# Optimization experiments

Hardware: AMD Instinct MI355X
Metric: run time of the kernel (lower is better)

The kernel has to match this reference:

```python
import jax, jax.numpy as jnp
import numpy as np

N_NODES = 50000
N_EDGES = 800000
NODE_DIM = 256
HIDDEN_DIM = 256
LN_EPS = 1e-5


def setup_inputs() -> dict:
    key = jax.random.key(0)
    ks = jax.random.split(key, 8)
    d, h = NODE_DIM, HIDDEN_DIM
    return {
        "node_features": jax.random.normal(ks[0], (N_NODES, d), jnp.float32),
        "src": jax.random.randint(ks[1], (N_EDGES,), 0, N_NODES, jnp.int32),
        "dst": jax.random.randint(ks[2], (N_EDGES,), 0, N_NODES, jnp.int32),
        "edge_weight": jax.random.uniform(ks[3], (N_EDGES,), jnp.float32),
        "W1": jax.random.normal(ks[4], (d, h), jnp.float32) / np.sqrt(d),
        "b1": jnp.zeros((h,), jnp.float32),
        "g1": jnp.ones((h,), jnp.float32),
        "be1": jnp.zeros((h,), jnp.float32),
        "W2": jax.random.normal(ks[5], (h, h), jnp.float32) / np.sqrt(h),
        "b2": jnp.zeros((h,), jnp.float32),
        "g2": jnp.ones((h,), jnp.float32),
        "be2": jnp.zeros((h,), jnp.float32),
        "Wp": jax.random.normal(ks[6], (h, d), jnp.float32) / np.sqrt(h),
        "bp": jnp.zeros((d,), jnp.float32),
    }


def _spmm(src, dst, w, x, n):
    # sparse adj @ x : agg[i] = sum_{edges e with dst=i} w_e * x[src_e]
    return jax.ops.segment_sum(w[:, None] * x[src], dst, num_segments=n)


def _layer_norm(x, g, b):
    mu = jnp.mean(x, -1, keepdims=True)
    var = jnp.mean(jnp.square(x - mu), -1, keepdims=True)
    return (x - mu) * jax.lax.rsqrt(var + LN_EPS) * g + b


def reference(node_features, src, dst, edge_weight, W1, b1, g1, be1, W2, b2, g2, be2, Wp, bp):
    n = node_features.shape[0]
    x = node_features
    for (W, b, g, be) in ((W1, b1, g1, be1), (W2, b2, g2, be2)):
        agg = _spmm(src, dst, edge_weight, x, n)
        h = (x + agg) @ W + b
        x = jax.nn.gelu(_layer_norm(h, g, be), approximate=False)
        # Dropout(0.1) is identity in eval mode
    return x @ Wp + bp
```

## Files before the change

### kernel.cpp

```cpp
#include <hip/hip_runtime.h>
#include <hip/hip_bf16.h>
#include <math.h>

#define N_NODES 50000
#define N_EDGES 800000
#define DIM 256
#define MPAD 50048
#define LN_EPS 1e-5f
#define SCAN_BLOCKS 196

typedef short bf16x8 __attribute__((ext_vector_type(8)));
typedef float f32x4 __attribute__((ext_vector_type(4)));
typedef unsigned short u16;
typedef u16 u16x8 __attribute__((ext_vector_type(8)));

__device__ __forceinline__ u16 f2bf(float f) {
    union { float f; unsigned u; } v; v.f = f;
    unsigned r = (v.u + 0x7FFFu + ((v.u >> 16) & 1u)) >> 16;
    return (u16)r;
}
__device__ __forceinline__ float bf2f(u16 h) {
    union { unsigned u; float f; } v; v.u = ((unsigned)h) << 16;
    return v.f;
}

__global__ void count_kernel(const int* __restrict__ dst, int* __restrict__ counts) {
    int e = blockIdx.x * 256 + threadIdx.x;
    if (e < N_EDGES) atomicAdd(&counts[dst[e]], 1);
}

__global__ void scan1_kernel(const int* __restrict__ counts, int* __restrict__ offsets,
                             int* __restrict__ bsum) {
    __shared__ int sh[256];
    int t = threadIdx.x;
    int idx = blockIdx.x * 256 + t;
    int v = (idx < N_NODES) ? counts[idx] : 0;
    sh[t] = v;
    __syncthreads();
#pragma unroll
    for (int off = 1; off < 256; off <<= 1) {
        int u = (t >= off) ? sh[t - off] : 0;
        __syncthreads();
        sh[t] += u;
        __syncthreads();
    }
    if (idx < N_NODES) offsets[idx] = sh[t] - v;
    if (t == 255) bsum[blockIdx.x] = sh[255];
}

__global__ void scan2_kernel(const int* __restrict__ bsum, int* __restrict__ bbase) {
    __shared__ int sh[256];
    int t = threadIdx.x;
    int v = (t < SCAN_BLOCKS) ? bsum[t] : 0;
    sh[t] = v;
    __syncthreads();
#pragma unroll
    for (int off = 1; off < 256; off <<= 1) {
        int u = (t >= off) ? sh[t - off] : 0;
        __syncthreads();
        sh[t] += u;
        __syncthreads();
    }
    if (t < SCAN_BLOCKS) bbase[t] = sh[t] - v;
}

__global__ void scan3_kernel(int* __restrict__ offsets, const int* __restrict__ bbase,
                             int* __restrict__ cursor) {
    int idx = blockIdx.x * 256 + threadIdx.x;
    if (idx < N_NODES) {
        int o = offsets[idx] + bbase[blockIdx.x];
        offsets[idx] = o;
        cursor[idx] = o;
    }
    if (idx == 0) offsets[N_NODES] = N_EDGES;
}

__global__ void scatter_kernel(const int* __restrict__ src, const int* __restrict__ dst,
                               const float* __restrict__ w, int* __restrict__ cursor,
                               int* __restrict__ sperm, float* __restrict__ wperm) {
    int e = blockIdx.x * 256 + threadIdx.x;
    if (e < N_EDGES) {
        int d = dst[e];
        int p = atomicAdd(&cursor[d], 1);
        sperm[p] = src[e];
        wperm[p] = w[e];
    }
}

__global__ void conv_kernel(const float* __restrict__ in, u16* __restrict__ out) {
    int i = blockIdx.x * 256 + threadIdx.x;
    float4 v = ((const float4*)in)[i];
    ushort4 o;
    o.x = f2bf(v.x); o.y = f2bf(v.y); o.z = f2bf(v.z); o.w = f2bf(v.w);
    ((ushort4*)out)[i] = o;
}

__global__ void convw_kernel(const float* __restrict__ W1, const float* __restrict__ W2,
                             const float* __restrict__ Wp, u16* __restrict__ WT) {
    int idx = blockIdx.x * 256 + threadIdx.x;
    int m = idx >> 16;
    int r = idx & 65535;
    int n = r >> 8, k = r & 255;
    const float* W = (m == 0) ? W1 : (m == 1) ? W2 : Wp;
    WT[idx] = f2bf(W[k * 256 + n]);
}

__global__ __launch_bounds__(256) void spmm_kernel(
        const u16* __restrict__ x, const int* __restrict__ offs,
        const int* __restrict__ sperm, const float* __restrict__ wperm,
        u16* __restrict__ y) {
    int wave = threadIdx.x >> 6;
    int lane = threadIdx.x & 63;
    int node = blockIdx.x * 4 + wave;
    if (node >= N_NODES) return;

    const ushort4* xv = (const ushort4*)x;
    ushort4 v = xv[(size_t)node * 64 + lane];
    float a0 = bf2f(v.x), a1 = bf2f(v.y), a2 = bf2f(v.z), a3 = bf2f(v.w);
    float b0 = 0, b1 = 0, b2 = 0, b3 = 0;
    float c0 = 0, c1 = 0, c2 = 0, c3 = 0;
    float d0 = 0, d1 = 0, d2 = 0, d3 = 0;

    int p = offs[node];
    int p1 = offs[node + 1];
    for (; p + 4 <= p1; p += 4) {
        int s0 = sperm[p], s1 = sperm[p + 1], s2 = sperm[p + 2], s3 = sperm[p + 3];
        float w0 = wperm[p], w1 = wperm[p + 1], w2 = wperm[p + 2], w3 = wperm[p + 3];
        ushort4 v0 = xv[(size_t)s0 * 64 + lane];
        ushort4 v1 = xv[(size_t)s1 * 64 + lane];
        ushort4 v2 = xv[(size_t)s2 * 64 + lane];
        ushort4 v3 = xv[(size_t)s3 * 64 + lane];
        a0 += w0 * bf2f(v0.x); a1 += w0 * bf2f(v0.y); a2 += w0 * bf2f(v0.z); a3 += w0 * bf2f(v0.w);
        b0 += w1 * bf2f(v1.x); b1 += w1 * bf2f(v1.y); b2 += w1 * bf2f(v1.z); b3 += w1 * bf2f(v1.w);
        c0 += w2 * bf2f(v2.x); c1 += w2 * bf2f(v2.y); c2 += w2 * bf2f(v2.z); c3 += w2 * bf2f(v2.w);
        d0 += w3 * bf2f(v3.x); d1 += w3 * bf2f(v3.y); d2 += w3 * bf2f(v3.z); d3 += w3 * bf2f(v3.w);
    }
    for (; p < p1; ++p) {
        int s = sperm[p];
        float w = wperm[p];
        ushort4 vv = xv[(size_t)s * 64 + lane];
        a0 += w * bf2f(vv.x); a1 += w * bf2f(vv.y); a2 += w * bf2f(vv.z); a3 += w * bf2f(vv.w);
    }
    a0 += b0 + c0 + d0; a1 += b1 + c1 + d1;
    a2 += b2 + c2 + d2; a3 += b3 + c3 + d3;
    ushort4 o;
    o.x = f2bf(a0); o.y = f2bf(a1); o.z = f2bf(a2); o.w = f2bf(a3);
    ((ushort4*)(y + (size_t)node * 256))[lane] = o;
}

template <int MODE>
__global__ __launch_bounds__(256, 2) void gemm_kernel(
        const u16* __restrict__ A, const u16* __restrict__ BT,
        const float* __restrict__ bias, const float* __restrict__ g,
        const float* __restrict__ be, u16* __restrict__ xb_out,
        float* __restrict__ f_out) {
    int tid = threadIdx.x;
    int wave = tid >> 6, lane = tid & 63;
    int quad = lane >> 4, l15 = lane & 15;
    int row0 = blockIdx.x * 128 + wave * 32;

    const u16* ga0 = A + (size_t)(row0 + l15) * 256 + quad * 8;
    const u16* ga1 = ga0 + 16 * 256;
    const u16* gb = BT + (size_t)l15 * 256 + quad * 8;

    f32x4 acc0[16], acc1[16];
#pragma unroll
    for (int t = 0; t < 16; ++t) { acc0[t] = {0.f, 0.f, 0.f, 0.f}; acc1[t] = {0.f, 0.f, 0.f, 0.f}; }

#pragma unroll 2
    for (int kb = 0; kb < 8; ++kb) {
        bf16x8 af0 = *(const bf16x8*)(ga0 + kb * 32);
        bf16x8 af1 = *(const bf16x8*)(ga1 + kb * 32);
#pragma unroll
        for (int t = 0; t < 16; ++t) {
            bf16x8 bf = *(const bf16x8*)(gb + (size_t)t * 4096 + kb * 32);
            acc0[t] = __builtin_amdgcn_mfma_f32_16x16x32_bf16(af0, bf, acc0[t], 0, 0, 0);
            acc1[t] = __builtin_amdgcn_mfma_f32_16x16x32_bf16(af1, bf, acc1[t], 0, 0, 0);
        }
    }

#pragma unroll
    for (int rf = 0; rf < 2; ++rf) {
        f32x4* acc = rf ? acc1 : acc0;
        int rbase = row0 + rf * 16 + quad * 4;
        if (MODE == 0) {
#pragma unroll
            for (int t = 0; t < 16; ++t) {
                float bv = bias[t * 16 + l15];
#pragma unroll
                for (int i = 0; i < 4; ++i) acc[t][i] += bv;
            }
#pragma unroll
            for (int i = 0; i < 4; ++i) {
                float s = 0.f, q = 0.f;
#pragma unroll
                for (int t = 0; t < 16; ++t) { float v = acc[t][i]; s += v; q += v * v; }
                for (int off = 1; off < 16; off <<= 1) {
                    s += __shfl_xor(s, off);
                    q += __shfl_xor(q, off);
                }
                float mu = s * (1.0f / 256.0f);
                float var = q * (1.0f / 256.0f) - mu * mu;
                float rs = rsqrtf(var + LN_EPS);
                int row = rbase + i;
#pragma unroll
                for (int t = 0; t < 16; ++t) {
                    int c = t * 16 + l15;
                    float v = (acc[t][i] - mu) * rs * g[c] + be[c];
                    float ge = 0.5f * v * (1.0f + erff(v * 0.70710678118f));
                    xb_out[(size_t)row * 256 + c] = f2bf(ge);
                }
            }
        } else {
#pragma unroll
            for (int i = 0; i < 4; ++i) {
                int row = rbase + i;
                if (row < N_NODES) {
#pragma unroll
                    for (int t = 0; t < 16; ++t) {
                        int c = t * 16 + l15;
                        f_out[(size_t)row * 256 + c] = acc[t][i] + bias[c];
                    }
                }
            }
        }
    }
}

extern "C" void kernel_launch(void* const* d_in, const int* in_sizes, int n_in,
                              void* d_out, int out_size, void* d_ws, size_t ws_size,
                              hipStream_t stream) {
    const float* nodef = (const float*)d_in[0];
    const int*   src   = (const int*)d_in[1];
    const int*   dst   = (const int*)d_in[2];
    const float* ew    = (const float*)d_in[3];
    const float* W1 = (const float*)d_in[4];
    const float* b1 = (const float*)d_in[5];
    const float* g1 = (const float*)d_in[6];
    const float* be1 = (const float*)d_in[7];
    const float* W2 = (const float*)d_in[8];
    const float* b2 = (const float*)d_in[9];
    const float* g2 = (const float*)d_in[10];
    const float* be2 = (const float*)d_in[11];
    const float* Wp = (const float*)d_in[12];
    const float* bp = (const float*)d_in[13];
    float* out = (float*)d_out;

    char* ws = (char*)d_ws;
    size_t off = 0;
    auto alloc = [&](size_t bytes) -> void* {
        void* p = ws + off;
        off += (bytes + 255) & ~(size_t)255;
        return p;
    };
    u16*   ybuf    = (u16*)alloc((size_t)MPAD * 256 * 2);
    u16*   xbuf    = (u16*)alloc((size_t)MPAD * 256 * 2);
    u16*   WT      = (u16*)alloc((size_t)3 * 65536 * 2);
    int*   counts  = (int*)alloc((size_t)N_NODES * 4);
    int*   offsets = (int*)alloc((size_t)(N_NODES + 1) * 4);
    int*   cursor  = (int*)alloc((size_t)N_NODES * 4);
    int*   sperm   = (int*)alloc((size_t)N_EDGES * 4);
    float* wperm   = (float*)alloc((size_t)N_EDGES * 4);
    int*   bsum    = (int*)alloc((size_t)SCAN_BLOCKS * 4);
    int*   bbase   = (int*)alloc((size_t)SCAN_BLOCKS * 4);

    hipMemsetAsync(counts, 0, (size_t)N_NODES * 4, stream);
    count_kernel<<<(N_EDGES + 255) / 256, 256, 0, stream>>>(dst, counts);
    scan1_kernel<<<SCAN_BLOCKS, 256, 0, stream>>>(counts, offsets, bsum);
    scan2_kernel<<<1, 256, 0, stream>>>(bsum, bbase);
    scan3_kernel<<<SCAN_BLOCKS, 256, 0, stream>>>(offsets, bbase, cursor);
    scatter_kernel<<<(N_EDGES + 255) / 256, 256, 0, stream>>>(src, dst, ew, cursor, sperm, wperm);
    conv_kernel<<<(N_NODES * 256 / 4) / 256, 256, 0, stream>>>(nodef, xbuf);
    convw_kernel<<<768, 256, 0, stream>>>(W1, W2, Wp, WT);

    const int GB = MPAD / 128;
    spmm_kernel<<<(N_NODES + 3) / 4, 256, 0, stream>>>(xbuf, offsets, sperm, wperm, ybuf);
    gemm_kernel<0><<<GB, 256, 0, stream>>>(ybuf, WT, b1, g1, be1, xbuf, nullptr);
    spmm_kernel<<<(N_NODES + 3) / 4, 256, 0, stream>>>(xbuf, offsets, sperm, wperm, ybuf);
    gemm_kernel<0><<<GB, 256, 0, stream>>>(ybuf, WT + 65536, b2, g2, be2, xbuf, nullptr);
    gemm_kernel<1><<<GB, 256, 0, stream>>>(xbuf, WT + 2 * 65536, bp, nullptr, nullptr, nullptr, out);
}
```

Baseline: 509.8 us.

## Write SpMM output in MFMA-tiled layout, stage weights in LDS, widen GEMM tiles

```diff
diff --git a/kernel.cpp b/kernel.cpp
--- a/kernel.cpp
+++ b/kernel.cpp
@@ -5,9 +5,10 @@
 #define N_NODES 50000
 #define N_EDGES 800000
 #define DIM 256
-#define MPAD 50048
+#define MPAD 50176
 #define LN_EPS 1e-5f
 #define SCAN_BLOCKS 196
+#define LDB 264
 
 typedef short bf16x8 __attribute__((ext_vector_type(8)));
 typedef float f32x4 __attribute__((ext_vector_type(4)));
@@ -22,6 +23,10 @@
 __device__ __forceinline__ float bf2f(u16 h) {
     union { unsigned u; float f; } v; v.u = ((unsigned)h) << 16;
     return v.f;
+}
+__device__ __forceinline__ float gelu_f(float x) {
+    float z = x * (1.595769122f + 0.0713548162726f * x * x);
+    return x * (1.0f / (1.0f + __expf(-z)));
 }
 
 __global__ void count_kernel(const int* __restrict__ dst, int* __restrict__ counts) {
@@ -109,92 +114,132 @@
         const u16* __restrict__ x, const int* __restrict__ offs,
         const int* __restrict__ sperm, const float* __restrict__ wperm,
         u16* __restrict__ y) {
-    int wave = threadIdx.x >> 6;
-    int lane = threadIdx.x & 63;
-    int node = blockIdx.x * 4 + wave;
-    if (node >= N_NODES) return;
+    __shared__ u16 tile[16 * 256];
+    int tid = threadIdx.x;
+    int wave = tid >> 6;
+    int lane = tid & 63;
+    int node0 = blockIdx.x * 16 + wave * 4;
 
     const ushort4* xv = (const ushort4*)x;
-    ushort4 v = xv[(size_t)node * 64 + lane];
-    float a0 = bf2f(v.x), a1 = bf2f(v.y), a2 = bf2f(v.z), a3 = bf2f(v.w);
-    float b0 = 0, b1 = 0, b2 = 0, b3 = 0;
-    float c0 = 0, c1 = 0, c2 = 0, c3 = 0;
-    float d0 = 0, d1 = 0, d2 = 0, d3 = 0;
-
-    int p = offs[node];
-    int p1 = offs[node + 1];
-    for (; p + 4 <= p1; p += 4) {
-        int s0 = sperm[p], s1 = sperm[p + 1], s2 = sperm[p + 2], s3 = sperm[p + 3];
-        float w0 = wperm[p], w1 = wperm[p + 1], w2 = wperm[p + 2], w3 = wperm[p + 3];
-        ushort4 v0 = xv[(size_t)s0 * 64 + lane];
-        ushort4 v1 = xv[(size_t)s1 * 64 + lane];
-        ushort4 v2 = xv[(size_t)s2 * 64 + lane];
-        ushort4 v3 = xv[(size_t)s3 * 64 + lane];
-        a0 += w0 * bf2f(v0.x); a1 += w0 * bf2f(v0.y); a2 += w0 * bf2f(v0.z); a3 += w0 * bf2f(v0.w);
-        b0 += w1 * bf2f(v1.x); b1 += w1 * bf2f(v1.y); b2 += w1 * bf2f(v1.z); b3 += w1 * bf2f(v1.w);
-        c0 += w2 * bf2f(v2.x); c1 += w2 * bf2f(v2.y); c2 += w2 * bf2f(v2.z); c3 += w2 * bf2f(v2.w);
-        d0 += w3 * bf2f(v3.x); d1 += w3 * bf2f(v3.y); d2 += w3 * bf2f(v3.z); d3 += w3 * bf2f(v3.w);
-    }
-    for (; p < p1; ++p) {
-        int s = sperm[p];
-        float w = wperm[p];
-        ushort4 vv = xv[(size_t)s * 64 + lane];
-        a0 += w * bf2f(vv.x); a1 += w * bf2f(vv.y); a2 += w * bf2f(vv.z); a3 += w * bf2f(vv.w);
-    }
-    a0 += b0 + c0 + d0; a1 += b1 + c1 + d1;
-    a2 += b2 + c2 + d2; a3 += b3 + c3 + d3;
-    ushort4 o;
-    o.x = f2bf(a0); o.y = f2bf(a1); o.z = f2bf(a2); o.w = f2bf(a3);
-    ((ushort4*)(y + (size_t)node * 256))[lane] = o;
-}
-
-template <int MODE>
-__global__ __launch_bounds__(256, 2) void gemm_kernel(
+#pragma unroll 1
+    for (int i = 0; i < 4; ++i) {
+        int node = node0 + i;
+        ushort4 v = xv[(size_t)node * 64 + lane];
+        float a0 = bf2f(v.x), a1 = bf2f(v.y), a2 = bf2f(v.z), a3 = bf2f(v.w);
+        float b0 = 0, b1 = 0, b2 = 0, b3 = 0;
+        float c0 = 0, c1 = 0, c2 = 0, c3 = 0;
+        float d0 = 0, d1 = 0, d2 = 0, d3 = 0;
+
+        int p = offs[node];
+        int p1 = offs[node + 1];
+        for (; p + 4 <= p1; p += 4) {
+            int s0 = sperm[p], s1 = sperm[p + 1], s2 = sperm[p + 2], s3 = sperm[p + 3];
+            float w0 = wperm[p], w1 = wperm[p + 1], w2 = wperm[p + 2], w3 = wperm[p + 3];
+            ushort4 v0 = xv[(size_t)s0 * 64 + lane];
+            ushort4 v1 = xv[(size_t)s1 * 64 + lane];
+            ushort4 v2 = xv[(size_t)s2 * 64 + lane];
+            ushort4 v3 = xv[(size_t)s3 * 64 + lane];
+            a0 += w0 * bf2f(v0.x); a1 += w0 * bf2f(v0.y); a2 += w0 * bf2f(v0.z); a3 += w0 * bf2f(v0.w);
+            b0 += w1 * bf2f(v1.x); b1 += w1 * bf2f(v1.y); b2 += w1 * bf2f(v1.z); b3 += w1 * bf2f(v1.w);
+            c0 += w2 * bf2f(v2.x); c1 += w2 * bf2f(v2.y); c2 += w2 * bf2f(v2.z); c3 += w2 * bf2f(v2.w);
+            d0 += w3 * bf2f(v3.x); d1 += w3 * bf2f(v3.y); d2 += w3 * bf2f(v3.z); d3 += w3 * bf2f(v3.w);
+        }
+        for (; p < p1; ++p) {
+            int s = sperm[p];
+            float w = wperm[p];
+            ushort4 vv = xv[(size_t)s * 64 + lane];
+            a0 += w * bf2f(vv.x); a1 += w * bf2f(vv.y); a2 += w * bf2f(vv.z); a3 += w * bf2f(vv.w);
+        }
+        a0 += b0 + c0 + d0; a1 += b1 + c1 + d1;
+        a2 += b2 + c2 + d2; a3 += b3 + c3 + d3;
+        ushort4 o;
+        o.x = f2bf(a0); o.y = f2bf(a1); o.z = f2bf(a2); o.w = f2bf(a3);
+        ((ushort4*)&tile[(wave * 4 + i) * 256])[lane] = o;
+    }
+    __syncthreads();
+    u16* outb = y + (size_t)blockIdx.x * 4096;
+#pragma unroll
+    for (int h = 0; h < 2; ++h) {
+        int gI = tid + h * 256;
+        int r = gI & 15;
+        int k0 = (gI >> 6) * 32 + ((gI >> 4) & 3) * 8;
+        u16x8 v = *(const u16x8*)&tile[r * 256 + k0];
+        *(u16x8*)(outb + (size_t)gI * 8) = v;
+    }
+}
+
+template <int MODE, int OUT_TILED>
+__global__ __launch_bounds__(256, 1) void gemm_kernel(
         const u16* __restrict__ A, const u16* __restrict__ BT,
         const float* __restrict__ bias, const float* __restrict__ g,
         const float* __restrict__ be, u16* __restrict__ xb_out,
         float* __restrict__ f_out) {
+    __shared__ u16 b_lds[256 * LDB];
     int tid = threadIdx.x;
     int wave = tid >> 6, lane = tid & 63;
     int quad = lane >> 4, l15 = lane & 15;
-    int row0 = blockIdx.x * 128 + wave * 32;
-
-    const u16* ga0 = A + (size_t)(row0 + l15) * 256 + quad * 8;
-    const u16* ga1 = ga0 + 16 * 256;
-    const u16* gb = BT + (size_t)l15 * 256 + quad * 8;
-
-    f32x4 acc0[16], acc1[16];
-#pragma unroll
-    for (int t = 0; t < 16; ++t) { acc0[t] = {0.f, 0.f, 0.f, 0.f}; acc1[t] = {0.f, 0.f, 0.f, 0.f}; }
-
-#pragma unroll 2
+
+#pragma unroll
+    for (int i = 0; i < 32; ++i) {
+        int c = i * 256 + tid;
+        u16x8 v = *(const u16x8*)(BT + (size_t)c * 8);
+        *(u16x8*)&b_lds[(c >> 5) * LDB + (c & 31) * 8] = v;
+    }
+
+    int tbase = blockIdx.x * 16 + wave * 4;
+    const u16* ga0 = A + (size_t)(tbase + 0) * 4096 + lane * 8;
+    const u16* ga1 = A + (size_t)(tbase + 1) * 4096 + lane * 8;
+    const u16* ga2 = A + (size_t)(tbase + 2) * 4096 + lane * 8;
+    const u16* ga3 = A + (size_t)(tbase + 3) * 4096 + lane * 8;
+    bf16x8 p0 = *(const bf16x8*)ga0;
+    bf16x8 p1 = *(const bf16x8*)ga1;
+    bf16x8 p2 = *(const bf16x8*)ga2;
+    bf16x8 p3 = *(const bf16x8*)ga3;
+
+    f32x4 acc[4][16];
+#pragma unroll
+    for (int rf = 0; rf < 4; ++rf)
+#pragma unroll
+        for (int t = 0; t < 16; ++t) acc[rf][t] = {0.f, 0.f, 0.f, 0.f};
+
+    __syncthreads();
+
+#pragma unroll
     for (int kb = 0; kb < 8; ++kb) {
-        bf16x8 af0 = *(const bf16x8*)(ga0 + kb * 32);
-        bf16x8 af1 = *(const bf16x8*)(ga1 + kb * 32);
+        bf16x8 a0 = p0, a1 = p1, a2 = p2, a3 = p3;
+        if (kb < 7) {
+            p0 = *(const bf16x8*)(ga0 + (kb + 1) * 512);
+            p1 = *(const bf16x8*)(ga1 + (kb + 1) * 512);
+            p2 = *(const bf16x8*)(ga2 + (kb + 1) * 512);
+            p3 = *(const bf16x8*)(ga3 + (kb + 1) * 512);
+        }
+        const u16* bl = &b_lds[l15 * LDB + kb * 32 + quad * 8];
 #pragma unroll
         for (int t = 0; t < 16; ++t) {
-            bf16x8 bf = *(const bf16x8*)(gb + (size_t)t * 4096 + kb * 32);
-            acc0[t] = __builtin_amdgcn_mfma_f32_16x16x32_bf16(af0, bf, acc0[t], 0, 0, 0);
-            acc1[t] = __builtin_amdgcn_mfma_f32_16x16x32_bf16(af1, bf, acc1[t], 0, 0, 0);
-        }
-    }
-
-#pragma unroll
-    for (int rf = 0; rf < 2; ++rf) {
-        f32x4* acc = rf ? acc1 : acc0;
-        int rbase = row0 + rf * 16 + quad * 4;
+            bf16x8 bf = *(const bf16x8*)(bl + t * 16 * LDB);
+            acc[0][t] = __builtin_amdgcn_mfma_f32_16x16x32_bf16(a0, bf, acc[0][t], 0, 0, 0);
+            acc[1][t] = __builtin_amdgcn_mfma_f32_16x16x32_bf16(a1, bf, acc[1][t], 0, 0, 0);
+            acc[2][t] = __builtin_amdgcn_mfma_f32_16x16x32_bf16(a2, bf, acc[2][t], 0, 0, 0);
+            acc[3][t] = __builtin_amdgcn_mfma_f32_16x16x32_bf16(a3, bf, acc[3][t], 0, 0, 0);
+        }
+    }
+
+    int rowblk = blockIdx.x * 256 + wave * 64;
+#pragma unroll
+    for (int rf = 0; rf < 4; ++rf) {
+        int rbase = rowblk + rf * 16 + quad * 4;
         if (MODE == 0) {
 #pragma unroll
             for (int t = 0; t < 16; ++t) {
                 float bv = bias[t * 16 + l15];
 #pragma unroll
-                for (int i = 0; i < 4; ++i) acc[t][i] += bv;
+                for (int i = 0; i < 4; ++i) acc[rf][t][i] += bv;
             }
 #pragma unroll
             for (int i = 0; i < 4; ++i) {
                 float s = 0.f, q = 0.f;
 #pragma unroll
-                for (int t = 0; t < 16; ++t) { float v = acc[t][i]; s += v; q += v * v; }
+                for (int t = 0; t < 16; ++t) { float v = acc[rf][t][i]; s += v; q += v * v; }
                 for (int off = 1; off < 16; off <<= 1) {
                     s += __shfl_xor(s, off);
                     q += __shfl_xor(q, off);
@@ -206,9 +251,15 @@
 #pragma unroll
                 for (int t = 0; t < 16; ++t) {
                     int c = t * 16 + l15;
-                    float v = (acc[t][i] - mu) * rs * g[c] + be[c];
-                    float ge = 0.5f * v * (1.0f + erff(v * 0.70710678118f));
-                    xb_out[(size_t)row * 256 + c] = f2bf(ge);
+                    float v = (acc[rf][t][i] - mu) * rs * g[c] + be[c];
+                    u16 ob = f2bf(gelu_f(v));
+                    if (OUT_TILED) {
+                        size_t o = (size_t)(row >> 4) * 4096 + (c >> 5) * 512 +
+                                   ((c >> 3) & 3) * 128 + (row & 15) * 8 + (c & 7);
+                        xb_out[o] = ob;
+                    } else {
+                        xb_out[(size_t)row * 256 + c] = ob;
+                    }
                 }
             }
         } else {
@@ -219,7 +270,7 @@
 #pragma unroll
                     for (int t = 0; t < 16; ++t) {
                         int c = t * 16 + l15;
-                        f_out[(size_t)row * 256 + c] = acc[t][i] + bias[c];
+                        f_out[(size_t)row * 256 + c] = acc[rf][t][i] + bias[c];
                     }
                 }
             }
@@ -270,13 +321,14 @@
     scan2_kernel<<<1, 256, 0, stream>>>(bsum, bbase);
     scan3_kernel<<<SCAN_BLOCKS, 256, 0, stream>>>(offsets, bbase, cursor);
     scatter_kernel<<<(N_EDGES + 255) / 256, 256, 0, stream>>>(src, dst, ew, cursor, sperm, wperm);
-    conv_kernel<<<(N_NODES * 256 / 4) / 256, 256, 0, stream>>>(nodef, xbuf);
+    conv_kernel<<<N_NODES * 64 / 256, 256, 0, stream>>>(nodef, xbuf);
     convw_kernel<<<768, 256, 0, stream>>>(W1, W2, Wp, WT);
 
-    const int GB = MPAD / 128;
-    spmm_kernel<<<(N_NODES + 3) / 4, 256, 0, stream>>>(xbuf, offsets, sperm, wperm, ybuf);
-    gemm_kernel<0><<<GB, 256, 0, stream>>>(ybuf, WT, b1, g1, be1, xbuf, nullptr);
-    spmm_kernel<<<(N_NODES + 3) / 4, 256, 0, stream>>>(xbuf, offsets, sperm, wperm, ybuf);
-    gemm_kernel<0><<<GB, 256, 0, stream>>>(ybuf, WT + 65536, b2, g2, be2, xbuf, nullptr);
-    gemm_kernel<1><<<GB, 256, 0, stream>>>(xbuf, WT + 2 * 65536, bp, nullptr, nullptr, nullptr, out);
-}
+    const int GB = MPAD / 256;
+    const int SB = N_NODES / 16;
+    spmm_kernel<<<SB, 256, 0, stream>>>(xbuf, offsets, sperm, wperm, ybuf);
+    gemm_kernel<0, 0><<<GB, 256, 0, stream>>>(ybuf, WT, b1, g1, be1, xbuf, nullptr);
+    spmm_kernel<<<SB, 256, 0, stream>>>(xbuf, offsets, sperm, wperm, ybuf);
+    gemm_kernel<0, 1><<<GB, 256, 0, stream>>>(ybuf, WT + 65536, b2, g2, be2, ybuf, nullptr);
+    gemm_kernel<1, 0><<<GB, 256, 0, stream>>>(ybuf, WT + 2 * 65536, bp, nullptr, nullptr, nullptr, out);
+}
```

Measured after the change: 447.7 us. 12.2% less time.
